# Optimization experiments

Hardware: AMD Instinct MI355X
Metric: run time of the kernel (lower is better)

Reference implementation:

```python
import jax, jax.numpy as jnp
import numpy as np

I, NH, HD = 768, 12, 64          # input_dim, head_num, per-head hidden
H = NH * HD                       # total LSTM hidden per direction (=768)
B, S = 64, 512


def _block_mask(in_per_head, hid_per_head, nh):
    # Replicates get_block_mask: block-diagonal per head, repeated for 4 gates.
    Ht = hid_per_head * nh
    m = np.zeros((4 * Ht, in_per_head * nh), np.float32)
    for h in range(nh):
        cs = slice(h * in_per_head, (h + 1) * in_per_head)
        for g in range(4):
            m[g * Ht + h * hid_per_head: g * Ht + (h + 1) * hid_per_head, cs] = 1.0
    return jnp.asarray(m)


def _head_mask(hid, nh):
    # block_diag of ones(hid,hid) per head, concatenated for fwd|bwd halves.
    bd = np.kron(np.eye(nh, dtype=np.float32), np.ones((hid, hid), np.float32))
    return jnp.asarray(np.concatenate([bd, bd], axis=1))


def setup_inputs() -> dict:
    key = jax.random.key(0)
    ks = jax.random.split(key, 16)
    s = 1.0 / np.sqrt(H)
    u = lambda k, shp: jax.random.uniform(k, shp, jnp.float32, -s, s)
    mask_ih = _block_mask(I // NH, HD, NH)   # [4H, I]
    mask_hh = _block_mask(HD, HD, NH)        # [4H, H]
    mask_head = _head_mask(HD, NH)           # [H, 2H]
    return {
        "x": jax.random.normal(ks[0], (B, S, I), jnp.float32),
        "pre_w": u(ks[1], (I, I)), "pre_b": u(ks[2], (I,)),
        "wih_f": u(ks[3], (4 * H, I)) * mask_ih,
        "whh_f": u(ks[4], (4 * H, H)) * mask_hh,
        "bih_f": u(ks[5], (4 * H,)), "bhh_f": u(ks[6], (4 * H,)),
        "wih_b": u(ks[7], (4 * H, I)) * mask_ih,
        "whh_b": u(ks[8], (4 * H, H)) * mask_hh,
        "bih_b": u(ks[9], (4 * H,)), "bhh_b": u(ks[10], (4 * H,)),
        "head_w": u(ks[11], (H, 2 * H)) * mask_head,
        "head_b": u(ks[12], (H,)),
        "post_w": u(ks[13], (I, H)), "post_b": u(ks[14], (I,)),
    }


def _lstm_dir(xs, wih, whh, bih, bhh):
    # xs: [B,S,I] -> hidden states [B,S,H]; torch gate order i,f,g,o
    xw = jnp.einsum('bsi,gi->bsg', xs, wih) + bih + bhh  # [B,S,4H]
    xw = jnp.swapaxes(xw, 0, 1)                           # [S,B,4H]
    Bv = xs.shape[0]
    Hv = whh.shape[1]

    def step(carry, xt):
        h, c = carry
        gates = xt + h @ whh.T
        i, f, g, o = jnp.split(gates, 4, axis=-1)
        c = jax.nn.sigmoid(f) * c + jax.nn.sigmoid(i) * jnp.tanh(g)
        h = jax.nn.sigmoid(o) * jnp.tanh(c)
        return (h, c), h

    init = (jnp.zeros((Bv, Hv), xs.dtype), jnp.zeros((Bv, Hv), xs.dtype))
    _, hs = jax.lax.scan(step, init, xw)
    return jnp.swapaxes(hs, 0, 1)


def reference(x, pre_w, pre_b, wih_f, whh_f, bih_f, bhh_f,
              wih_b, whh_b, bih_b, bhh_b, head_w, head_b, post_w, post_b):
    x = x @ pre_w.T + pre_b                                   # pre_proj
    hf = _lstm_dir(x, wih_f, whh_f, bih_f, bhh_f)             # forward dir
    hb = jnp.flip(_lstm_dir(jnp.flip(x, 1), wih_b, whh_b, bih_b, bhh_b), 1)
    lstm_out = jnp.concatenate([hf, hb], axis=-1)             # [B,S,2H]
    lstm_out = lstm_out @ head_w.T + head_b                   # head_proj [B,S,H]
    out = lstm_out @ post_w.T + post_b                        # post_proj [B,S,I]
    return (out, lstm_out)
```

## Files before the change

### kernel.cpp

```cpp
#include <hip/hip_runtime.h>
#include <stdint.h>

typedef __attribute__((ext_vector_type(8))) short short8;
typedef __attribute__((ext_vector_type(4))) float f32x4;

__device__ __forceinline__ ushort f2bf(float f) {
    uint u = __float_as_uint(f);
    u += 0x7FFF + ((u >> 16) & 1);
    return (ushort)(u >> 16);
}

#define GLDS16(g, l)                                                  \
    __builtin_amdgcn_global_load_lds(                                 \
        (__attribute__((address_space(1))) void*)(g),                 \
        (__attribute__((address_space(3))) void*)(l), 16, 0, 0)

__global__ void prep_w(const float* __restrict__ pre_w, const float* __restrict__ post_w,
                       const float* __restrict__ wih_f, const float* __restrict__ whh_f,
                       const float* __restrict__ wih_b, const float* __restrict__ whh_b,
                       const float* __restrict__ head_w,
                       ushort* __restrict__ prewb, ushort* __restrict__ postwb,
                       ushort* __restrict__ wcat, ushort* __restrict__ wcat2) {
    int i = blockIdx.x * 256 + threadIdx.x;
    const int NW = 589824;
    if (i < NW) { prewb[i] = f2bf(pre_w[i]); return; }
    i -= NW;
    if (i < NW) { postwb[i] = f2bf(post_w[i]); return; }
    i -= NW;
    if (i < 786432) {
        int k = i & 127, n = (i >> 7) & 255, dh = i >> 15;
        int d = dh / 12, h = dh % 12;
        int gr = (n >> 6) * 768 + h * 64 + (n & 63);
        const float* wih = d ? wih_b : wih_f;
        const float* whh = d ? whh_b : whh_f;
        float v = (k < 64) ? wih[gr * 768 + h * 64 + k] : whh[gr * 768 + h * 64 + (k - 64)];
        wcat[i] = f2bf(v); return;
    }
    i -= 786432;
    {
        int k = i & 127, n = (i >> 7) & 63, h = i >> 13;
        int row = h * 64 + n;
        float v = (k < 64) ? head_w[row * 1536 + h * 64 + k]
                           : head_w[row * 1536 + 768 + h * 64 + (k - 64)];
        wcat2[i] = f2bf(v);
    }
}

template<int INF32, int OUTBF>
__global__ __launch_bounds__(256) void gemm_bt(const void* __restrict__ Ain,
                                               const ushort* __restrict__ Bt,
                                               const float* __restrict__ bias,
                                               void* __restrict__ out) {
    __shared__ __align__(16) ushort sA[128 * 64];
    __shared__ __align__(16) ushort sB[128 * 64];
    int t = threadIdx.x;
    int m0 = blockIdx.x * 128, n0 = blockIdx.y * 128;
    int w = t >> 6, l = t & 63, r = l & 15, q = l >> 4;
    int wm = w >> 1, wn = w & 1;
    f32x4 acc[4][4];
#pragma unroll
    for (int a = 0; a < 4; ++a)
#pragma unroll
        for (int b = 0; b < 4; ++b) acc[a][b] = (f32x4){0.f, 0.f, 0.f, 0.f};

    for (int kt = 0; kt < 12; ++kt) {
        int k0 = kt * 64;
        __syncthreads();
#pragma unroll
        for (int i = 0; i < 4; ++i) {
            int c = t + i * 256, row = c >> 3, col = (c & 7) * 8;
            GLDS16(&Bt[(size_t)(n0 + row) * 768 + k0 + col], &sB[row * 64 + col]);
        }
        if (INF32) {
#pragma unroll
            for (int i = 0; i < 4; ++i) {
                int c = t + i * 256, row = c >> 3, col = (c & 7) * 8;
                const float* ap = (const float*)Ain + (size_t)(m0 + row) * 768 + k0 + col;
                float4 u0 = *(const float4*)ap;
                float4 u1 = *(const float4*)(ap + 4);
                short8 v;
                v[0] = (short)f2bf(u0.x); v[1] = (short)f2bf(u0.y);
                v[2] = (short)f2bf(u0.z); v[3] = (short)f2bf(u0.w);
                v[4] = (short)f2bf(u1.x); v[5] = (short)f2bf(u1.y);
                v[6] = (short)f2bf(u1.z); v[7] = (short)f2bf(u1.w);
                *(short8*)&sA[row * 64 + col] = v;
            }
        } else {
#pragma unroll
            for (int i = 0; i < 4; ++i) {
                int c = t + i * 256, row = c >> 3, col = (c & 7) * 8;
                GLDS16(&((const ushort*)Ain)[(size_t)(m0 + row) * 768 + k0 + col],
                       &sA[row * 64 + col]);
            }
        }
        __syncthreads();
#pragma unroll
        for (int kk = 0; kk < 2; ++kk) {
            short8 af[4], bf[4];
#pragma unroll
            for (int mt = 0; mt < 4; ++mt)
                af[mt] = *(const short8*)&sA[(wm * 64 + mt * 16 + r) * 64 + kk * 32 + q * 8];
#pragma unroll
            for (int nt = 0; nt < 4; ++nt)
                bf[nt] = *(const short8*)&sB[(wn * 64 + nt * 16 + r) * 64 + kk * 32 + q * 8];
#pragma unroll
            for (int mt = 0; mt < 4; ++mt)
#pragma unroll
                for (int nt = 0; nt < 4; ++nt)
                    acc[mt][nt] = __builtin_amdgcn_mfma_f32_16x16x32_bf16(af[mt], bf[nt], acc[mt][nt], 0, 0, 0);
        }
    }
#pragma unroll
    for (int nt = 0; nt < 4; ++nt) {
        int col = n0 + wn * 64 + nt * 16 + r;
        float bv = bias[col];
#pragma unroll
        for (int mt = 0; mt < 4; ++mt) {
            int rowb = m0 + wm * 64 + mt * 16 + q * 4;
#pragma unroll
            for (int j = 0; j < 4; ++j) {
                float v = acc[mt][nt][j] + bv;
                if (OUTBF) ((ushort*)out)[(size_t)(rowb + j) * 768 + col] = f2bf(v);
                else       ((float*)out)[(size_t)(rowb + j) * 768 + col] = v;
            }
        }
    }
}

__global__ __launch_bounds__(512) void lstm_rec(const ushort* __restrict__ ybf,
                                                const ushort* __restrict__ wcat,
                                                const float* __restrict__ bih_f,
                                                const float* __restrict__ bhh_f,
                                                const float* __restrict__ bih_b,
                                                const float* __restrict__ bhh_b,
                                                ushort* __restrict__ hs) {
    __shared__ __align__(16) float gbuf[256 * 20];
    __shared__ __align__(16) ushort hbuf[16 * 64];
    int t = threadIdx.x;
    int w = t >> 6, l = t & 63, r = l & 15, q = l >> 4;
    int b0 = blockIdx.x * 16, h = blockIdx.y, d = blockIdx.z;

    const ushort* wp = wcat + (size_t)(d * 12 + h) * 256 * 128;
    short8 bfr[2][4];
#pragma unroll
    for (int nt = 0; nt < 2; ++nt)
#pragma unroll
        for (int kk = 0; kk < 4; ++kk) {
            int n = w * 32 + nt * 16 + r, k = kk * 32 + q * 8;
            bfr[nt][kk] = *(const short8*)&wp[n * 128 + k];
        }
    const float* bih = d ? bih_b : bih_f;
    const float* bhh = d ? bhh_b : bhh_f;
    float bv[2];
#pragma unroll
    for (int nt = 0; nt < 2; ++nt) {
        int n = w * 32 + nt * 16 + r;
        int gr = (n >> 6) * 768 + h * 64 + (n & 63);
        bv[nt] = bih[gr] + bhh[gr];
    }
    int bl = t & 15, j2 = t >> 4;
    float cst[2] = {0.f, 0.f};
    ((uint*)hbuf)[t] = 0u;

    const ushort* yrow = ybf + (size_t)(b0 + r) * 512 * 768 + h * 64 + q * 8;
    int s = d ? 511 : 0;
    int sstep = d ? -1 : 1;
    short8 yf0 = *(const short8*)&yrow[s * 768];
    short8 yf1 = *(const short8*)&yrow[s * 768 + 32];
    __syncthreads();

    for (int it = 0; it < 512; ++it) {
        short8 yc0 = yf0, yc1 = yf1;
        int snext = s + sstep;
        if (it < 511) {
            yf0 = *(const short8*)&yrow[snext * 768];
            yf1 = *(const short8*)&yrow[snext * 768 + 32];
        }
        short8 ah0 = *(const short8*)&hbuf[r * 64 + ((q ^ (r & 7)) * 8)];
        short8 ah1 = *(const short8*)&hbuf[r * 64 + (((4 + q) ^ (r & 7)) * 8)];
        f32x4 acc[2];
#pragma unroll
        for (int nt = 0; nt < 2; ++nt) {
            f32x4 a = (f32x4){bv[nt], bv[nt], bv[nt], bv[nt]};
            a = __builtin_amdgcn_mfma_f32_16x16x32_bf16(yc0, bfr[nt][0], a, 0, 0, 0);
            a = __builtin_amdgcn_mfma_f32_16x16x32_bf16(yc1, bfr[nt][1], a, 0, 0, 0);
            a = __builtin_amdgcn_mfma_f32_16x16x32_bf16(ah0, bfr[nt][2], a, 0, 0, 0);
            a = __builtin_amdgcn_mfma_f32_16x16x32_bf16(ah1, bfr[nt][3], a, 0, 0, 0);
            acc[nt] = a;
        }
#pragma unroll
        for (int nt = 0; nt < 2; ++nt) {
            int n = w * 32 + nt * 16 + r;
            *(f32x4*)&gbuf[n * 20 + q * 4] = acc[nt];
        }
        __syncthreads();
        float hh[2];
#pragma unroll
        for (int jj = 0; jj < 2; ++jj) {
            int j = 2 * j2 + jj;
            float ip = gbuf[j * 20 + bl];
            float fp = gbuf[(64 + j) * 20 + bl];
            float gp = gbuf[(128 + j) * 20 + bl];
            float op = gbuf[(192 + j) * 20 + bl];
            float ig = 1.f / (1.f + __expf(-ip));
            float fg = 1.f / (1.f + __expf(-fp));
            float gg = 2.f / (1.f + __expf(-2.f * gp)) - 1.f;
            float og = 1.f / (1.f + __expf(-op));
            float c = fg * cst[jj] + ig * gg;
            cst[jj] = c;
            float th = 2.f / (1.f + __expf(-2.f * c)) - 1.f;
            hh[jj] = og * th;
        }
        {
            int j0 = 2 * j2, g8 = j0 >> 3;
            uint pk = (uint)f2bf(hh[0]) | ((uint)f2bf(hh[1]) << 16);
            *(uint*)&hbuf[bl * 64 + ((g8 ^ (bl & 7)) * 8 + (j0 & 7))] = pk;
        }
        __syncthreads();
        if (t < 256) {
            int rr = t >> 4, c16 = t & 15;
            int jj0 = c16 * 4, gg8 = c16 >> 1;
            uint2 v = *(const uint2*)&hbuf[rr * 64 + ((gg8 ^ (rr & 7)) * 8 + (jj0 & 7))];
            *(uint2*)&hs[((size_t)(b0 + rr) * 512 + s) * 1536 + d * 768 + h * 64 + jj0] = v;
        }
        s = snext;
    }
}

__global__ __launch_bounds__(256) void head_proj(const ushort* __restrict__ hs,
                                                 const ushort* __restrict__ wcat2,
                                                 const float* __restrict__ head_b,
                                                 float* __restrict__ out2,
                                                 ushort* __restrict__ out1b) {
    __shared__ __align__(16) ushort sA[128 * 128];
    __shared__ __align__(16) ushort sB[64 * 128];
    int t = threadIdx.x;
    int h = blockIdx.y, m0 = blockIdx.x * 128;
#pragma unroll
    for (int i = 0; i < 8; ++i) {
        int c = t + i * 256, row = c >> 4, c16 = c & 15;
        int dd = c16 >> 3, kc = (c16 & 7) * 8;
        GLDS16(&hs[(size_t)(m0 + row) * 1536 + dd * 768 + h * 64 + kc],
               &sA[row * 128 + c16 * 8]);
    }
#pragma unroll
    for (int i = 0; i < 4; ++i) {
        int c = t + i * 256, row = c >> 4, kc = (c & 15) * 8;
        GLDS16(&wcat2[(size_t)(h * 64 + row) * 128 + kc], &sB[row * 128 + kc]);
    }
    __syncthreads();
    int w = t >> 6, l = t & 63, r = l & 15, q = l >> 4;
    f32x4 acc[2][4];
#pragma unroll
    for (int a = 0; a < 2; ++a)
#pragma unroll
        for (int b = 0; b < 4; ++b) acc[a][b] = (f32x4){0.f, 0.f, 0.f, 0.f};
#pragma unroll
    for (int kk = 0; kk < 4; ++kk) {
        short8 af[2], bf[4];
#pragma unroll
        for (int mt = 0; mt < 2; ++mt)
            af[mt] = *(const short8*)&sA[(w * 32 + mt * 16 + r) * 128 + kk * 32 + q * 8];
#pragma unroll
        for (int nt = 0; nt < 4; ++nt)
            bf[nt] = *(const short8*)&sB[(nt * 16 + r) * 128 + kk * 32 + q * 8];
#pragma unroll
        for (int mt = 0; mt < 2; ++mt)
#pragma unroll
            for (int nt = 0; nt < 4; ++nt)
                acc[mt][nt] = __builtin_amdgcn_mfma_f32_16x16x32_bf16(af[mt], bf[nt], acc[mt][nt], 0, 0, 0);
    }
#pragma unroll
    for (int nt = 0; nt < 4; ++nt) {
        int colg = h * 64 + nt * 16 + r;
        float bvv = head_b[colg];
#pragma unroll
        for (int mt = 0; mt < 2; ++mt) {
            int rowb = m0 + w * 32 + mt * 16 + q * 4;
#pragma unroll
            for (int j = 0; j < 4; ++j) {
                float v = acc[mt][nt][j] + bvv;
                out2[(size_t)(rowb + j) * 768 + colg] = v;
                out1b[(size_t)(rowb + j) * 768 + colg] = f2bf(v);
            }
        }
    }
}

extern "C" void kernel_launch(void* const* d_in, const int* in_sizes, int n_in,
                              void* d_out, int out_size, void* d_ws, size_t ws_size,
                              hipStream_t stream) {
    const float* x      = (const float*)d_in[0];
    const float* pre_w  = (const float*)d_in[1];
    const float* pre_b  = (const float*)d_in[2];
    const float* wih_f  = (const float*)d_in[3];
    const float* whh_f  = (const float*)d_in[4];
    const float* bih_f  = (const float*)d_in[5];
    const float* bhh_f  = (const float*)d_in[6];
    const float* wih_b  = (const float*)d_in[7];
    const float* whh_b  = (const float*)d_in[8];
    const float* bih_b  = (const float*)d_in[9];
    const float* bhh_b  = (const float*)d_in[10];
    const float* head_w = (const float*)d_in[11];
    const float* head_b = (const float*)d_in[12];
    const float* post_w = (const float*)d_in[13];
    const float* post_b = (const float*)d_in[14];

    char* ws = (char*)d_ws;
    ushort* ybf    = (ushort*)(ws + 0);
    ushort* hsb    = (ushort*)(ws + 50331648);
    ushort* wcat   = (ushort*)(ws + 150994944);
    ushort* wcat2  = (ushort*)(ws + 152567808);
    ushort* prewb  = (ushort*)(ws + 152764416);
    ushort* postwb = (ushort*)(ws + 153944064);

    float* outp  = (float*)d_out;
    float* out2p = outp + 25165824;
    ushort* out1b = ybf;

    prep_w<<<dim3(8064), dim3(256), 0, stream>>>(pre_w, post_w, wih_f, whh_f,
                                                 wih_b, whh_b, head_w,
                                                 prewb, postwb, wcat, wcat2);
    gemm_bt<1, 1><<<dim3(256, 6), dim3(256), 0, stream>>>(x, prewb, pre_b, (void*)ybf);
    lstm_rec<<<dim3(4, 12, 2), dim3(512), 0, stream>>>(ybf, wcat, bih_f, bhh_f,
                                                       bih_b, bhh_b, hsb);
    head_proj<<<dim3(256, 12), dim3(256), 0, stream>>>(hsb, wcat2, head_b, out2p, out1b);
    gemm_bt<0, 0><<<dim3(256, 6), dim3(256), 0, stream>>>(out1b, postwb, post_b, (void*)outp);
}
```

Baseline: 1.010 ms.

## Keep LSTM gates in registers via shuffles and double-buffer hidden state

Reorders the packed recurrent weights so each lane and its xor-8 partner hold complementary gates. Gate activations are then exchanged with warp shuffles instead of a shared-memory gate buffer. The hidden-state buffer is double-buffered, so each timestep needs one barrier instead of two. The input-projection MFMAs for the next step are computed ahead and off the recurrent critical path, and sigmoid/tanh use a fast reciprocal. This adds more register pressure and slightly less accurate activations.

```diff
diff --git a/kernel.cpp b/kernel.cpp
--- a/kernel.cpp
+++ b/kernel.cpp
@@ -3,11 +3,19 @@
 
 typedef __attribute__((ext_vector_type(8))) short short8;
 typedef __attribute__((ext_vector_type(4))) float f32x4;
+
+#define MFMA __builtin_amdgcn_mfma_f32_16x16x32_bf16
 
 __device__ __forceinline__ ushort f2bf(float f) {
     uint u = __float_as_uint(f);
     u += 0x7FFF + ((u >> 16) & 1);
     return (ushort)(u >> 16);
+}
+__device__ __forceinline__ float sigm(float x) {
+    return __builtin_amdgcn_rcpf(1.f + __expf(-x));
+}
+__device__ __forceinline__ float tanh2(float x) {
+    return 1.f - 2.f * __builtin_amdgcn_rcpf(1.f + __expf(2.f * x));
 }
 
 #define GLDS16(g, l)                                                  \
@@ -30,7 +38,9 @@
     if (i < 786432) {
         int k = i & 127, n = (i >> 7) & 255, dh = i >> 15;
         int d = dh / 12, h = dh % 12;
-        int gr = (n >> 6) * 768 + h * 64 + (n & 63);
+        int g = ((n >> 4) & 1) * 2 + ((n >> 3) & 1);
+        int j = ((n >> 5) << 3) + (n & 7);
+        int gr = g * 768 + h * 64 + j;
         const float* wih = d ? wih_b : wih_f;
         const float* whh = d ? whh_b : whh_f;
         float v = (k < 64) ? wih[gr * 768 + h * 64 + k] : whh[gr * 768 + h * 64 + (k - 64)];
@@ -107,7 +117,7 @@
             for (int mt = 0; mt < 4; ++mt)
 #pragma unroll
                 for (int nt = 0; nt < 4; ++nt)
-                    acc[mt][nt] = __builtin_amdgcn_mfma_f32_16x16x32_bf16(af[mt], bf[nt], acc[mt][nt], 0, 0, 0);
+                    acc[mt][nt] = MFMA(af[mt], bf[nt], acc[mt][nt], 0, 0, 0);
         }
     }
 #pragma unroll
@@ -134,96 +144,113 @@
                                                 const float* __restrict__ bih_b,
                                                 const float* __restrict__ bhh_b,
                                                 ushort* __restrict__ hs) {
-    __shared__ __align__(16) float gbuf[256 * 20];
-    __shared__ __align__(16) ushort hbuf[16 * 64];
+    __shared__ __align__(16) ushort hbuf[2][16 * 64];
     int t = threadIdx.x;
     int w = t >> 6, l = t & 63, r = l & 15, q = l >> 4;
     int b0 = blockIdx.x * 16, h = blockIdx.y, d = blockIdx.z;
 
     const ushort* wp = wcat + (size_t)(d * 12 + h) * 256 * 128;
-    short8 bfr[2][4];
+    short8 by[2][2], bh[2][2];
 #pragma unroll
     for (int nt = 0; nt < 2; ++nt)
 #pragma unroll
-        for (int kk = 0; kk < 4; ++kk) {
-            int n = w * 32 + nt * 16 + r, k = kk * 32 + q * 8;
-            bfr[nt][kk] = *(const short8*)&wp[n * 128 + k];
+        for (int kk = 0; kk < 2; ++kk) {
+            int n = w * 32 + nt * 16 + r;
+            by[nt][kk] = *(const short8*)&wp[n * 128 + kk * 32 + q * 8];
+            bh[nt][kk] = *(const short8*)&wp[n * 128 + 64 + kk * 32 + q * 8];
         }
     const float* bih = d ? bih_b : bih_f;
     const float* bhh = d ? bhh_b : bhh_f;
     float bv[2];
 #pragma unroll
     for (int nt = 0; nt < 2; ++nt) {
-        int n = w * 32 + nt * 16 + r;
-        int gr = (n >> 6) * 768 + h * 64 + (n & 63);
+        int g = nt * 2 + (r >> 3), j = w * 8 + (r & 7);
+        int gr = g * 768 + h * 64 + j;
         bv[nt] = bih[gr] + bhh[gr];
     }
-    int bl = t & 15, j2 = t >> 4;
+    bool lo = (r < 8);
+    int j0 = lo ? 0 : 2;
     float cst[2] = {0.f, 0.f};
     ((uint*)hbuf)[t] = 0u;
 
     const ushort* yrow = ybf + (size_t)(b0 + r) * 512 * 768 + h * 64 + q * 8;
-    int s = d ? 511 : 0;
-    int sstep = d ? -1 : 1;
-    short8 yf0 = *(const short8*)&yrow[s * 768];
-    short8 yf1 = *(const short8*)&yrow[s * 768 + 32];
+    int s0 = d ? 511 : 0, st = d ? -1 : 1;
+
+    short8 ya0 = *(const short8*)&yrow[s0 * 768];
+    short8 ya1 = *(const short8*)&yrow[s0 * 768 + 32];
+    f32x4 accy0 = (f32x4){bv[0], bv[0], bv[0], bv[0]};
+    f32x4 accy1 = (f32x4){bv[1], bv[1], bv[1], bv[1]};
+    accy0 = MFMA(ya0, by[0][0], accy0, 0, 0, 0);
+    accy0 = MFMA(ya1, by[0][1], accy0, 0, 0, 0);
+    accy1 = MFMA(ya0, by[1][0], accy1, 0, 0, 0);
+    accy1 = MFMA(ya1, by[1][1], accy1, 0, 0, 0);
+    short8 yb0 = *(const short8*)&yrow[(s0 + st) * 768];
+    short8 yb1 = *(const short8*)&yrow[(s0 + st) * 768 + 32];
     __syncthreads();
 
-    for (int it = 0; it < 512; ++it) {
-        short8 yc0 = yf0, yc1 = yf1;
-        int snext = s + sstep;
-        if (it < 511) {
-            yf0 = *(const short8*)&yrow[snext * 768];
-            yf1 = *(const short8*)&yrow[snext * 768 + 32];
-        }
-        short8 ah0 = *(const short8*)&hbuf[r * 64 + ((q ^ (r & 7)) * 8)];
-        short8 ah1 = *(const short8*)&hbuf[r * 64 + (((4 + q) ^ (r & 7)) * 8)];
-        f32x4 acc[2];
-#pragma unroll
-        for (int nt = 0; nt < 2; ++nt) {
-            f32x4 a = (f32x4){bv[nt], bv[nt], bv[nt], bv[nt]};
-            a = __builtin_amdgcn_mfma_f32_16x16x32_bf16(yc0, bfr[nt][0], a, 0, 0, 0);
-            a = __builtin_amdgcn_mfma_f32_16x16x32_bf16(yc1, bfr[nt][1], a, 0, 0, 0);
-            a = __builtin_amdgcn_mfma_f32_16x16x32_bf16(ah0, bfr[nt][2], a, 0, 0, 0);
-            a = __builtin_amdgcn_mfma_f32_16x16x32_bf16(ah1, bfr[nt][3], a, 0, 0, 0);
-            acc[nt] = a;
-        }
-#pragma unroll
-        for (int nt = 0; nt < 2; ++nt) {
-            int n = w * 32 + nt * 16 + r;
-            *(f32x4*)&gbuf[n * 20 + q * 4] = acc[nt];
-        }
-        __syncthreads();
-        float hh[2];
-#pragma unroll
-        for (int jj = 0; jj < 2; ++jj) {
-            int j = 2 * j2 + jj;
-            float ip = gbuf[j * 20 + bl];
-            float fp = gbuf[(64 + j) * 20 + bl];
-            float gp = gbuf[(128 + j) * 20 + bl];
-            float op = gbuf[(192 + j) * 20 + bl];
-            float ig = 1.f / (1.f + __expf(-ip));
-            float fg = 1.f / (1.f + __expf(-fp));
-            float gg = 2.f / (1.f + __expf(-2.f * gp)) - 1.f;
-            float og = 1.f / (1.f + __expf(-op));
-            float c = fg * cst[jj] + ig * gg;
-            cst[jj] = c;
-            float th = 2.f / (1.f + __expf(-2.f * c)) - 1.f;
-            hh[jj] = og * th;
-        }
-        {
-            int j0 = 2 * j2, g8 = j0 >> 3;
-            uint pk = (uint)f2bf(hh[0]) | ((uint)f2bf(hh[1]) << 16);
-            *(uint*)&hbuf[bl * 64 + ((g8 ^ (bl & 7)) * 8 + (j0 & 7))] = pk;
-        }
-        __syncthreads();
-        if (t < 256) {
+    auto body = [&](int it, short8& yc0, short8& yc1, short8& yn0, short8& yn1) {
+        int cur = it & 1;
+        int s = s0 + it * st;
+        if (it > 0 && t < 256) {
             int rr = t >> 4, c16 = t & 15;
             int jj0 = c16 * 4, gg8 = c16 >> 1;
-            uint2 v = *(const uint2*)&hbuf[rr * 64 + ((gg8 ^ (rr & 7)) * 8 + (jj0 & 7))];
-            *(uint2*)&hs[((size_t)(b0 + rr) * 512 + s) * 1536 + d * 768 + h * 64 + jj0] = v;
-        }
-        s = snext;
+            uint2 v = *(const uint2*)&hbuf[cur][rr * 64 + ((gg8 ^ (rr & 7)) * 8 + (jj0 & 7))];
+            *(uint2*)&hs[((size_t)(b0 + rr) * 512 + (s - st)) * 1536 + d * 768 + h * 64 + jj0] = v;
+        }
+        short8 ah0 = *(const short8*)&hbuf[cur][r * 64 + ((q ^ (r & 7)) * 8)];
+        short8 ah1 = *(const short8*)&hbuf[cur][r * 64 + (((4 + q) ^ (r & 7)) * 8)];
+        if (it < 510) {
+            yn0 = *(const short8*)&yrow[(s + 2 * st) * 768];
+            yn1 = *(const short8*)&yrow[(s + 2 * st) * 768 + 32];
+        }
+        f32x4 a0 = accy0, a1 = accy1;
+        a0 = MFMA(ah0, bh[0][0], a0, 0, 0, 0);
+        a0 = MFMA(ah1, bh[0][1], a0, 0, 0, 0);
+        a1 = MFMA(ah0, bh[1][0], a1, 0, 0, 0);
+        a1 = MFMA(ah1, bh[1][1], a1, 0, 0, 0);
+        float e0[4], e1[4];
+#pragma unroll
+        for (int m = 0; m < 4; ++m) {
+            e0[m] = __shfl_xor(a0[m], 8);
+            e1[m] = __shfl_xor(a1[m], 8);
+        }
+        float hh[2];
+#pragma unroll
+        for (int k = 0; k < 2; ++k) {
+            int m = j0 + k;
+            float ip = lo ? a0[m] : e0[m];
+            float fp = lo ? e0[m] : a0[m];
+            float gp = lo ? a1[m] : e1[m];
+            float op = lo ? e1[m] : a1[m];
+            float ig = sigm(ip), fg = sigm(fp), og = sigm(op);
+            float gg = tanh2(gp);
+            float c = fg * cst[k] + ig * gg;
+            cst[k] = c;
+            hh[k] = og * tanh2(c);
+        }
+        int nxt = cur ^ 1;
+        int ro = 4 * q + j0;
+        hbuf[nxt][ro * 64 + ((w ^ (ro & 7)) * 8) + (r & 7)] = f2bf(hh[0]);
+        int ro1 = ro + 1;
+        hbuf[nxt][ro1 * 64 + ((w ^ (ro1 & 7)) * 8) + (r & 7)] = f2bf(hh[1]);
+        accy0 = (f32x4){bv[0], bv[0], bv[0], bv[0]};
+        accy1 = (f32x4){bv[1], bv[1], bv[1], bv[1]};
+        accy0 = MFMA(yc0, by[0][0], accy0, 0, 0, 0);
+        accy0 = MFMA(yc1, by[0][1], accy0, 0, 0, 0);
+        accy1 = MFMA(yc0, by[1][0], accy1, 0, 0, 0);
+        accy1 = MFMA(yc1, by[1][1], accy1, 0, 0, 0);
+        __syncthreads();
+    };
+
+    for (int itb = 0; itb < 512; itb += 2) {
+        body(itb, yb0, yb1, ya0, ya1);
+        body(itb + 1, ya0, ya1, yb0, yb1);
+    }
+    if (t < 256) {
+        int rr = t >> 4, c16 = t & 15;
+        int jj0 = c16 * 4, gg8 = c16 >> 1;
+        uint2 v = *(const uint2*)&hbuf[0][rr * 64 + ((gg8 ^ (rr & 7)) * 8 + (jj0 & 7))];
+        *(uint2*)&hs[((size_t)(b0 + rr) * 512 + (s0 + 511 * st)) * 1536 + d * 768 + h * 64 + jj0] = v;
     }
 }
 
@@ -268,7 +295,7 @@
         for (int mt = 0; mt < 2; ++mt)
 #pragma unroll
             for (int nt = 0; nt < 4; ++nt)
-                acc[mt][nt] = __builtin_amdgcn_mfma_f32_16x16x32_bf16(af[mt], bf[nt], acc[mt][nt], 0, 0, 0);
+                acc[mt][nt] = MFMA(af[mt], bf[nt], acc[mt][nt], 0, 0, 0);
     }
 #pragma unroll
     for (int nt = 0; nt < 4; ++nt) {
```

Measured after the change: 860.5 us. 1.17x faster.
